# Performance work log

Hardware: AMD Instinct MI355X
Metric: run time of the kernel (lower is better)

The kernel has to match this reference:

```python
import math
import jax, jax.numpy as jnp
import numpy as np

N_HEAD = 16
N_HEAD_KV = 4
HEAD_DIM = 64
WINDOW = 512  # (window, 0) sliding-window causal, as in flash_attn window_size
ROPE_BASE = 10000.0


def _rope(x):
    """Rotate-half RoPE. x: (B, T, H, D)."""
    T, D = x.shape[1], x.shape[3]
    half = D // 2
    inv_freq = 1.0 / (ROPE_BASE ** (jnp.arange(half, dtype=jnp.float32) / half))
    ang = jnp.arange(T, dtype=jnp.float32)[:, None] * inv_freq[None, :]  # (T, half)
    cos = jnp.concatenate([jnp.cos(ang), jnp.cos(ang)], axis=-1)[None, :, None, :]
    sin = jnp.concatenate([jnp.sin(ang), jnp.sin(ang)], axis=-1)[None, :, None, :]
    x1, x2 = jnp.split(x, 2, axis=-1)
    rot = jnp.concatenate([-x2, x1], axis=-1)
    return x * cos.astype(x.dtype) + rot * sin.astype(x.dtype)


def setup_inputs() -> dict:
    key = jax.random.key(0)
    ks = jax.random.split(key, 7)
    B, T, C = 2, 2048, 1024
    Ckv = N_HEAD_KV * HEAD_DIM
    x = jax.random.normal(ks[0], (B, T, C), dtype=jnp.float32)
    seq_lengths = jax.random.randint(ks[1], (B,), T // 2, T + 1, dtype=jnp.int32)
    s = 0.02
    Wq = jax.random.normal(ks[2], (C, C), dtype=jnp.float32) * s
    Wk = jax.random.normal(ks[3], (C, Ckv), dtype=jnp.float32) * s
    Wv = jax.random.normal(ks[4], (C, Ckv), dtype=jnp.float32) * s
    Wo = jax.random.normal(ks[5], (C, C), dtype=jnp.float32) * s
    return {"x": x, "seq_lengths": seq_lengths, "Wq": Wq, "Wk": Wk, "Wv": Wv, "Wo": Wo}


def reference(x, seq_lengths, Wq, Wk, Wv, Wo):
    B, T, C = x.shape
    scale = 1.0 / math.sqrt(HEAD_DIM)
    q = (x @ Wq).reshape(B, T, N_HEAD, HEAD_DIM)
    k = (x @ Wk).reshape(B, T, N_HEAD_KV, HEAD_DIM)
    v = (x @ Wv).reshape(B, T, N_HEAD_KV, HEAD_DIM)
    q = _rope(q)
    k = _rope(k)
    # GQA: repeat_interleave KV heads up to N_HEAD
    rep = N_HEAD // N_HEAD_KV
    k = jnp.repeat(k, rep, axis=2)
    v = jnp.repeat(v, rep, axis=2)
    scores = jnp.einsum("bqhd,bkhd->bhqk", q, k) * scale  # (B,H,T,T)
    pos = jnp.arange(T)
    causal = pos[None, :] <= pos[:, None]                      # k <= q
    window = pos[None, :] >= (pos[:, None] - WINDOW)           # k >= q - W
    key_valid = pos[None, :] < seq_lengths[:, None]            # (B,T)
    mask = (causal & window)[None, None, :, :] & key_valid[:, None, None, :]
    scores = jnp.where(mask, scores, jnp.float32(-1e9))
    attn = jax.nn.softmax(scores, axis=-1)
    out = jnp.einsum("bhqk,bkhd->bqhd", attn, v)
    # padded query positions are zeroed (pad_input semantics in the varlen path)
    q_valid = (pos[None, :] < seq_lengths[:, None]).astype(out.dtype)
    out = out * q_valid[:, :, None, None]
    return out.reshape(B, T, C) @ Wo
```

## Files before the change

kernel.cpp:

```cpp
#include <hip/hip_runtime.h>


using bf16x8 = __attribute__((ext_vector_type(8))) short;
using f32x4  = __attribute__((ext_vector_type(4))) float;

#define B_   2
#define T_   2048
#define H_   16
#define HKV_ 4
#define D_   64
#define WIN_ 512

#define QSCALE_ 0.18033688011112042f
#define LOG2_1E4_OVER32_ 0.41524101186092029f

__device__ __forceinline__ unsigned short f2b(float f) {
  union { float f; unsigned u; } v; v.f = f;
  unsigned r = v.u + 0x7FFFu + ((v.u >> 16) & 1u);
  return (unsigned short)(r >> 16);
}
__device__ __forceinline__ unsigned short f2b_fast(float f) {
  union { float f; unsigned u; } v; v.f = f;
  return (unsigned short)((v.u + 0x8000u) >> 16);
}

typedef const __attribute__((address_space(1))) void* gas_ptr;
typedef __attribute__((address_space(3))) void* las_ptr;
__device__ __forceinline__ void gl_lds16(const void* g, void* l) {
  __builtin_amdgcn_global_load_lds((gas_ptr)g, (las_ptr)l, 16, 0, 0);
}

__global__ __launch_bounds__(256) void prep_kernel(
    const float* __restrict__ x,
    const float* __restrict__ Wq, const float* __restrict__ Wk,
    const float* __restrict__ Wv, const float* __restrict__ Wo,
    unsigned short* __restrict__ xb,
    unsigned short* __restrict__ wqT, unsigned short* __restrict__ wkT,
    unsigned short* __restrict__ wvT, unsigned short* __restrict__ woT) {
  int bx = blockIdx.x;
  if (bx < 4096) {
    int i = bx * 256 + threadIdx.x;
    float4 v = ((const float4*)x)[i];
    ushort4 o; o.x = f2b(v.x); o.y = f2b(v.y); o.z = f2b(v.z); o.w = f2b(v.w);
    ((ushort4*)xb)[i] = o;
    return;
  }
  int id = bx - 4096;
  const float* W; unsigned short* WT; int N, n0, k0;
  if (id < 1024)      { W = Wq; WT = wqT; N = 1024; }
  else if (id < 2048) { W = Wo; WT = woT; N = 1024; id -= 1024; }
  else if (id < 2304) { W = Wk; WT = wkT; N = 256;  id -= 2048; }
  else                { W = Wv; WT = wvT; N = 256;  id -= 2304; }
  if (N == 1024) { n0 = (id & 31) * 32; k0 = (id >> 5) * 32; }
  else           { n0 = (id & 7)  * 32; k0 = (id >> 3) * 32; }
  __shared__ float tile[32][33];
  int tx = threadIdx.x & 31, ty = threadIdx.x >> 5;
#pragma unroll
  for (int yy = 0; yy < 32; yy += 8)
    tile[ty + yy][tx] = W[(size_t)(k0 + ty + yy) * N + n0 + tx];
  __syncthreads();
#pragma unroll
  for (int yy = 0; yy < 32; yy += 8)
    WT[(size_t)(n0 + ty + yy) * 1024 + k0 + tx] = f2b(tile[tx][ty + yy]);
}

__global__ __launch_bounds__(256) void gemm_qkv(
    const unsigned short* __restrict__ A,
    const unsigned short* __restrict__ WqT,
    const unsigned short* __restrict__ WkT,
    const unsigned short* __restrict__ WvT,
    unsigned short* __restrict__ qb,
    unsigned short* __restrict__ kbuf,
    unsigned short* __restrict__ vbT) {
  const int K = 1024;
  __shared__ unsigned short lA[2][64 * 32];
  __shared__ unsigned short lB[2][128 * 32];
  int tid = threadIdx.x, l = tid & 63, w = tid >> 6;
  int wr = w >> 1, wc = w & 1;
  int m0 = blockIdx.x * 64;
  int n0 = blockIdx.y * 128;
  const unsigned short* Bt; int nloc;
  if (n0 < 1024)      { Bt = WqT; nloc = n0; }
  else if (n0 < 1280) { Bt = WkT; nloc = n0 - 1024; }
  else                { Bt = WvT; nloc = n0 - 1280; }

  f32x4 acc[2][4] = {};

  const unsigned short* ga = A  + (size_t)(m0   + w * 16 + (l >> 2)) * K + (l & 3) * 8;
  const unsigned short* gb = Bt + (size_t)(nloc + w * 16 + (l >> 2)) * K + (l & 3) * 8;

#define STG(BUF, KOFF)                                                        \
  { gl_lds16(ga + (KOFF),                  &lA[BUF][w * 512]);                \
    gl_lds16(gb + (KOFF),                  &lB[BUF][w * 512]);                \
    gl_lds16(gb + (size_t)64 * K + (KOFF), &lB[BUF][w * 512 + 2048]); }

  STG(0, 0)
  __syncthreads();
  for (int k0 = 0; k0 < K; k0 += 32) {
    int buf = (k0 >> 5) & 1;
    if (k0 + 32 < K) STG(buf ^ 1, k0 + 32)
    bf16x8 af[2], bfr[4];
#pragma unroll
    for (int mf = 0; mf < 2; ++mf)
      af[mf] = *(const bf16x8*)(&lA[buf][(wr * 32 + mf * 16 + (l & 15)) * 32 + (l >> 4) * 8]);
#pragma unroll
    for (int nf = 0; nf < 4; ++nf)
      bfr[nf] = *(const bf16x8*)(&lB[buf][(wc * 64 + nf * 16 + (l & 15)) * 32 + (l >> 4) * 8]);
#pragma unroll
    for (int mf = 0; mf < 2; ++mf)
#pragma unroll
      for (int nf = 0; nf < 4; ++nf)
        acc[mf][nf] = __builtin_amdgcn_mfma_f32_16x16x32_bf16(af[mf], bfr[nf], acc[mf][nf], 0, 0, 0);
    __syncthreads();
  }
#undef STG

  int colbase = n0 + wc * 64;
  int rowbase = m0 + wr * 32;

  if (n0 < 1280) {
    float qs = (n0 < 1024) ? QSCALE_ : 1.0f;
#pragma unroll
    for (int nf = 0; nf < 2; ++nf) {
      int dd = nf * 16 + (l & 15);
      float inv = exp2f(-(float)dd * LOG2_1E4_OVER32_);
#pragma unroll
      for (int mf = 0; mf < 2; ++mf) {
#pragma unroll
        for (int i = 0; i < 4; ++i) {
          int t = (rowbase + mf * 16 + ((l >> 4) << 2) + i) & 2047;
          float sn, cs;
          __sincosf((float)t * inv, &sn, &cs);
          float x1 = acc[mf][nf][i], x2 = acc[mf][nf + 2][i];
          acc[mf][nf][i]     = (x1 * cs - x2 * sn) * qs;
          acc[mf][nf + 2][i] = (x2 * cs + x1 * sn) * qs;
        }
      }
    }
  }

#pragma unroll
  for (int mf = 0; mf < 2; ++mf)
#pragma unroll
    for (int nf = 0; nf < 4; ++nf) {
      int n    = colbase + nf * 16 + (l & 15);
      int mrow = rowbase + mf * 16 + ((l >> 4) << 2);
      int b = mrow >> 11, t = mrow & 2047;
      if (n < 1024) {
        int h = n >> 6, d = n & 63;
        size_t base = ((size_t)(b * 16 + h) * 2048 + t) * 64 + d;
#pragma unroll
        for (int i = 0; i < 4; ++i) qb[base + (size_t)i * 64] = f2b(acc[mf][nf][i]);
      } else if (n < 1280) {
        int hh = (n - 1024) >> 6, d = n & 63;
        size_t base = ((size_t)(b * 4 + hh) * 2048 + t) * 64 + d;
#pragma unroll
        for (int i = 0; i < 4; ++i) kbuf[base + (size_t)i * 64] = f2b(acc[mf][nf][i]);
      } else {
        int hh = (n - 1280) >> 6, d = n & 63;
        size_t base = ((size_t)((b * 4 + hh) * 64 + d)) * 2048 + t;
        ushort4 pk;
        pk.x = f2b(acc[mf][nf][0]); pk.y = f2b(acc[mf][nf][1]);
        pk.z = f2b(acc[mf][nf][2]); pk.w = f2b(acc[mf][nf][3]);
        *(ushort4*)(&vbT[base]) = pk;
      }
    }
}

__global__ __launch_bounds__(512, 4) void attn_kernel(
    const unsigned short* __restrict__ qb,
    const unsigned short* __restrict__ kb,
    const unsigned short* __restrict__ vbT,
    const int* __restrict__ seqlen,
    unsigned short* __restrict__ att) {
  __shared__ unsigned short kl[2][64 * 64];
  __shared__ unsigned short vt[2][64 * 64];
  __shared__ unsigned short pl[8][16 * 68];

  int bx = blockIdx.x;
  int g  = bx & 7;
  int wi = bx >> 3;
  int b  = g >> 2;
  int hk = g & 3;
  int h  = hk * 4 + (wi & 3);
  int qt = wi >> 2;
  int tid = threadIdx.x, l = tid & 63, w = tid >> 6;
  int q0 = qt << 7;
  int r0 = q0 + w * 16;
  int slen = seqlen[b];

  const unsigned short* qbase = qb  + ((size_t)(b * 16 + h)  * 2048) * 64;
  const unsigned short* kbase = kb  + ((size_t)(b * 4  + hk) * 2048) * 64;
  const unsigned short* vbase = vbT + ((size_t)(b * 4  + hk) * 64)   * 2048;

  bf16x8 aq[2];
#pragma unroll
  for (int s = 0; s < 2; ++s)
    aq[s] = *(const bf16x8*)(qbase + (size_t)(r0 + (l & 15)) * 64 + s * 32 + (l >> 4) * 8);

  f32x4 o[4] = {};
  float lp[4] = {0.f, 0.f, 0.f, 0.f};

  int lo = q0 >= WIN_ ? q0 - WIN_ : 0;
  int nt = (q0 + 128 - lo) >> 6;

  int srow = (w << 3) + (l >> 3);
  int scol = (((l & 7) ^ (l >> 3)) << 3);
  const unsigned short* ksrc = kbase + (size_t)srow * 64   + scol;
  const unsigned short* vsrc = vbase + (size_t)srow * 2048 + scol;

#define STAGE(BUF, KB0)                                                        \
  {                                                                            \
    gl_lds16(ksrc + (size_t)(KB0) * 64, &kl[BUF][w * 512]);                    \
    gl_lds16(vsrc + (KB0),              &vt[BUF][w * 512]);                    \
  }

  STAGE(0, lo)
  __syncthreads();

  for (int it = 0; it < nt; ++it) {
    int kb0 = lo + (it << 6);
    int cur = it & 1;
    if (it + 1 < nt) STAGE(cur ^ 1, kb0 + 64)

    if (kb0 <= r0 + 15 && kb0 + 63 >= r0 - WIN_) {
      f32x4 sa[4];
      __builtin_amdgcn_s_setprio(1);
#pragma unroll
      for (int nf = 0; nf < 4; ++nf) {
        int row = nf * 16 + (l & 15);
        const unsigned short* kp0 =
            &kl[cur][row * 64 + (((l >> 4)       ^ (l & 7)) << 3)];
        const unsigned short* kp1 =
            &kl[cur][row * 64 + (((4 + (l >> 4)) ^ (l & 7)) << 3)];
        f32x4 z = {};
        z = __builtin_amdgcn_mfma_f32_16x16x32_bf16(aq[0], *(const bf16x8*)kp0, z, 0, 0, 0);
        z = __builtin_amdgcn_mfma_f32_16x16x32_bf16(aq[1], *(const bf16x8*)kp1, z, 0, 0, 0);
        sa[nf] = z;
      }
      __builtin_amdgcn_s_setprio(0);

      bool noMask = (kb0 + 63 <= r0) && (kb0 >= r0 - 497);
      if (!noMask) {
#pragma unroll
        for (int nf = 0; nf < 4; ++nf) {
          int key = kb0 + nf * 16 + (l & 15);
#pragma unroll
          for (int i = 0; i < 4; ++i) {
            int qr = r0 + (l >> 4) * 4 + i;
            sa[nf][i] = (key <= qr && key >= qr - WIN_) ? sa[nf][i] : -1e30f;
          }
        }
      }

#pragma unroll
      for (int nf = 0; nf < 4; ++nf)
#pragma unroll
        for (int i = 0; i < 4; ++i) {
          float p = exp2f(sa[nf][i]);
          lp[i] += p;
          pl[w][((l >> 4) * 4 + i) * 68 + nf * 16 + (l & 15)] = f2b_fast(p);
        }

      bf16x8 ap0 = *(const bf16x8*)(&pl[w][(l & 15) * 68 + (l >> 4) * 8]);
      bf16x8 ap1 = *(const bf16x8*)(&pl[w][(l & 15) * 68 + 32 + (l >> 4) * 8]);

      __builtin_amdgcn_s_setprio(1);
#pragma unroll
      for (int df = 0; df < 4; ++df) {
        int row = df * 16 + (l & 15);
        const unsigned short* vp0 =
            &vt[cur][row * 64 + (((l >> 4)       ^ (l & 7)) << 3)];
        const unsigned short* vp1 =
            &vt[cur][row * 64 + (((4 + (l >> 4)) ^ (l & 7)) << 3)];
        o[df] = __builtin_amdgcn_mfma_f32_16x16x32_bf16(ap0, *(const bf16x8*)vp0, o[df], 0, 0, 0);
        o[df] = __builtin_amdgcn_mfma_f32_16x16x32_bf16(ap1, *(const bf16x8*)vp1, o[df], 0, 0, 0);
      }
      __builtin_amdgcn_s_setprio(0);
    }
    __syncthreads();
  }
#undef STAGE

#pragma unroll
  for (int off = 1; off <= 8; off <<= 1)
#pragma unroll
    for (int i = 0; i < 4; ++i)
      lp[i] += __shfl_xor(lp[i], off);

#pragma unroll
  for (int i = 0; i < 4; ++i) {
    int r = r0 + (l >> 4) * 4 + i;
    float inv = (r < slen && lp[i] > 0.f) ? 1.0f / lp[i] : 0.f;
#pragma unroll
    for (int df = 0; df < 4; ++df)
      att[((size_t)(b * 2048 + r)) * 1024 + h * 64 + df * 16 + (l & 15)] =
          f2b(o[df][i] * inv);
  }
}

__global__ __launch_bounds__(256) void gemm_out(
    const unsigned short* __restrict__ A,
    const unsigned short* __restrict__ Bt,
    float* __restrict__ C) {
  const int K = 1024;
  __shared__ unsigned short lA[2][64 * 32];
  __shared__ unsigned short lB[2][128 * 32];
  int tid = threadIdx.x, l = tid & 63, w = tid >> 6;
  int wr = w >> 1, wc = w & 1;
  int m0 = blockIdx.x * 64;
  int n0 = blockIdx.y * 128;

  f32x4 acc[2][4] = {};

  const unsigned short* ga = A  + (size_t)(m0 + w * 16 + (l >> 2)) * K + (l & 3) * 8;
  const unsigned short* gb = Bt + (size_t)(n0 + w * 16 + (l >> 2)) * K + (l & 3) * 8;

#define STG(BUF, KOFF)                                                        \
  { gl_lds16(ga + (KOFF),                  &lA[BUF][w * 512]);                \
    gl_lds16(gb + (KOFF),                  &lB[BUF][w * 512]);                \
    gl_lds16(gb + (size_t)64 * K + (KOFF), &lB[BUF][w * 512 + 2048]); }

  STG(0, 0)
  __syncthreads();
  for (int k0 = 0; k0 < K; k0 += 32) {
    int buf = (k0 >> 5) & 1;
    if (k0 + 32 < K) STG(buf ^ 1, k0 + 32)
    bf16x8 af[2], bfr[4];
#pragma unroll
    for (int mf = 0; mf < 2; ++mf)
      af[mf] = *(const bf16x8*)(&lA[buf][(wr * 32 + mf * 16 + (l & 15)) * 32 + (l >> 4) * 8]);
#pragma unroll
    for (int nf = 0; nf < 4; ++nf)
      bfr[nf] = *(const bf16x8*)(&lB[buf][(wc * 64 + nf * 16 + (l & 15)) * 32 + (l >> 4) * 8]);
#pragma unroll
    for (int mf = 0; mf < 2; ++mf)
#pragma unroll
      for (int nf = 0; nf < 4; ++nf)
        acc[mf][nf] = __builtin_amdgcn_mfma_f32_16x16x32_bf16(af[mf], bfr[nf], acc[mf][nf], 0, 0, 0);
    __syncthreads();
  }
#undef STG

  int colbase = n0 + wc * 64;
  int rowbase = m0 + wr * 32;
#pragma unroll
  for (int mf = 0; mf < 2; ++mf)
#pragma unroll
    for (int nf = 0; nf < 4; ++nf) {
      int n    = colbase + nf * 16 + (l & 15);
      int mrow = rowbase + mf * 16 + ((l >> 4) << 2);
#pragma unroll
      for (int i = 0; i < 4; ++i)
        C[(size_t)(mrow + i) * 1024 + n] = acc[mf][nf][i];
    }
}

extern "C" void kernel_launch(void* const* d_in, const int* in_sizes, int n_in,
                              void* d_out, int out_size, void* d_ws, size_t ws_size,
                              hipStream_t stream) {
  const float* x  = (const float*)d_in[0];
  const int*   sl = (const int*)d_in[1];
  const float* Wq = (const float*)d_in[2];
  const float* Wk = (const float*)d_in[3];
  const float* Wv = (const float*)d_in[4];
  const float* Wo = (const float*)d_in[5];
  float* out = (float*)d_out;

  char* p = (char*)d_ws;
  unsigned short* xb  = (unsigned short*)p; p += (size_t)4096 * 1024 * 2;
  unsigned short* wqT = (unsigned short*)p; p += (size_t)1024 * 1024 * 2;
  unsigned short* wkT = (unsigned short*)p; p += (size_t)256  * 1024 * 2;
  unsigned short* wvT = (unsigned short*)p; p += (size_t)256  * 1024 * 2;
  unsigned short* woT = (unsigned short*)p; p += (size_t)1024 * 1024 * 2;
  unsigned short* qb  = (unsigned short*)p; p += (size_t)B_ * H_   * T_ * D_ * 2;
  unsigned short* kbf = (unsigned short*)p; p += (size_t)B_ * HKV_ * T_ * D_ * 2;
  unsigned short* vbT = (unsigned short*)p; p += (size_t)B_ * HKV_ * D_ * T_ * 2;
  unsigned short* att = (unsigned short*)p; p += (size_t)4096 * 1024 * 2;

  prep_kernel<<<6656, 256, 0, stream>>>(x, Wq, Wk, Wv, Wo, xb, wqT, wkT, wvT, woT);
  gemm_qkv<<<dim3(64, 12), 256, 0, stream>>>(xb, wqT, wkT, wvT, qb, kbf, vbT);
  attn_kernel<<<512, 512, 0, stream>>>(qb, kbf, vbT, sl, att);
  gemm_out<<<dim3(64, 8), 256, 0, stream>>>(att, woT, out);
}
```

Baseline: 86.28 us.

## Deepen GEMM K-tile to 64 with XOR-swizzled LDS and explicit vmcnt pipelining

Both the QKV and output GEMMs now stage 64-wide K slices instead of 32, halving the number of loop iterations and barriers. The LDS layout gets an XOR swizzle on 16-byte chunks to avoid bank conflicts on the wider rows. Prefetch waits use explicit s_waitcnt vmcnt counts instead of a full __syncthreads, and s_setprio raises priority around the MFMA block. LDS usage doubles, which may lower occupancy, and the hand-tuned waitcnt relies on the compiler not reordering the async loads.

Result: faster. 69.47 us (-19.5%).

```diff
diff --git a/kernel.cpp b/kernel.cpp
--- a/kernel.cpp
+++ b/kernel.cpp
@@ -73,8 +73,8 @@
     unsigned short* __restrict__ kbuf,
     unsigned short* __restrict__ vbT) {
   const int K = 1024;
-  __shared__ unsigned short lA[2][64 * 32];
-  __shared__ unsigned short lB[2][128 * 32];
+  __shared__ unsigned short lA[2][64 * 64];
+  __shared__ unsigned short lB[2][128 * 64];
   int tid = threadIdx.x, l = tid & 63, w = tid >> 6;
   int wr = w >> 1, wc = w & 1;
   int m0 = blockIdx.x * 64;
@@ -86,32 +86,58 @@
 
   f32x4 acc[2][4] = {};
 
-  const unsigned short* ga = A  + (size_t)(m0   + w * 16 + (l >> 2)) * K + (l & 3) * 8;
-  const unsigned short* gb = Bt + (size_t)(nloc + w * 16 + (l >> 2)) * K + (l & 3) * 8;
-
-#define STG(BUF, KOFF)                                                        \
-  { gl_lds16(ga + (KOFF),                  &lA[BUF][w * 512]);                \
-    gl_lds16(gb + (KOFF),                  &lB[BUF][w * 512]);                \
-    gl_lds16(gb + (size_t)64 * K + (KOFF), &lB[BUF][w * 512 + 2048]); }
+  int scol = (((l & 7) ^ (l >> 3)) << 3);
+  const unsigned short* ga = A  + (size_t)(m0   + w * 16 + (l >> 3)) * K + scol;
+  const unsigned short* gb = Bt + (size_t)(nloc + w * 32 + (l >> 3)) * K + scol;
+
+#define STG(BUF, KOFF)                                                         \
+  {                                                                            \
+    gl_lds16(ga + (KOFF),                  &lA[BUF][(w * 16) * 64]);           \
+    gl_lds16(ga + 8 * K + (KOFF),          &lA[BUF][(w * 16 + 8) * 64]);       \
+    _Pragma("unroll")                                                          \
+    for (int j = 0; j < 4; ++j)                                                \
+      gl_lds16(gb + j * 8 * K + (KOFF),    &lB[BUF][(w * 32 + j * 8) * 64]);   \
+  }
 
   STG(0, 0)
-  __syncthreads();
-  for (int k0 = 0; k0 < K; k0 += 32) {
-    int buf = (k0 >> 5) & 1;
-    if (k0 + 32 < K) STG(buf ^ 1, k0 + 32)
-    bf16x8 af[2], bfr[4];
+  for (int it = 0; it < 16; ++it) {
+    int buf = it & 1;
+    if (it < 15) {
+      STG(buf ^ 1, (it + 1) * 64)
+      asm volatile("s_waitcnt vmcnt(6)" ::: "memory");
+    } else {
+      asm volatile("s_waitcnt vmcnt(0)" ::: "memory");
+    }
+    __builtin_amdgcn_sched_barrier(0);
+    __builtin_amdgcn_s_barrier();
+
+    bf16x8 af[2][2], bfr[4][2];
+#pragma unroll
+    for (int mf = 0; mf < 2; ++mf) {
+      int row = wr * 32 + mf * 16 + (l & 15);
+#pragma unroll
+      for (int ks = 0; ks < 2; ++ks)
+        af[mf][ks] = *(const bf16x8*)(
+            &lA[buf][row * 64 + (((ks * 4 + (l >> 4)) ^ (row & 7)) << 3)]);
+    }
+#pragma unroll
+    for (int nf = 0; nf < 4; ++nf) {
+      int row = wc * 64 + nf * 16 + (l & 15);
+#pragma unroll
+      for (int ks = 0; ks < 2; ++ks)
+        bfr[nf][ks] = *(const bf16x8*)(
+            &lB[buf][row * 64 + (((ks * 4 + (l >> 4)) ^ (row & 7)) << 3)]);
+    }
+    __builtin_amdgcn_s_setprio(1);
 #pragma unroll
     for (int mf = 0; mf < 2; ++mf)
-      af[mf] = *(const bf16x8*)(&lA[buf][(wr * 32 + mf * 16 + (l & 15)) * 32 + (l >> 4) * 8]);
-#pragma unroll
-    for (int nf = 0; nf < 4; ++nf)
-      bfr[nf] = *(const bf16x8*)(&lB[buf][(wc * 64 + nf * 16 + (l & 15)) * 32 + (l >> 4) * 8]);
-#pragma unroll
-    for (int mf = 0; mf < 2; ++mf)
-#pragma unroll
-      for (int nf = 0; nf < 4; ++nf)
-        acc[mf][nf] = __builtin_amdgcn_mfma_f32_16x16x32_bf16(af[mf], bfr[nf], acc[mf][nf], 0, 0, 0);
-    __syncthreads();
+#pragma unroll
+      for (int nf = 0; nf < 4; ++nf) {
+        acc[mf][nf] = __builtin_amdgcn_mfma_f32_16x16x32_bf16(af[mf][0], bfr[nf][0], acc[mf][nf], 0, 0, 0);
+        acc[mf][nf] = __builtin_amdgcn_mfma_f32_16x16x32_bf16(af[mf][1], bfr[nf][1], acc[mf][nf], 0, 0, 0);
+      }
+    __builtin_amdgcn_s_setprio(0);
+    __builtin_amdgcn_s_barrier();
   }
 #undef STG
 
@@ -304,8 +330,8 @@
     const unsigned short* __restrict__ Bt,
     float* __restrict__ C) {
   const int K = 1024;
-  __shared__ unsigned short lA[2][64 * 32];
-  __shared__ unsigned short lB[2][128 * 32];
+  __shared__ unsigned short lA[2][64 * 64];
+  __shared__ unsigned short lB[2][128 * 64];
   int tid = threadIdx.x, l = tid & 63, w = tid >> 6;
   int wr = w >> 1, wc = w & 1;
   int m0 = blockIdx.x * 64;
@@ -313,32 +339,58 @@
 
   f32x4 acc[2][4] = {};
 
-  const unsigned short* ga = A  + (size_t)(m0 + w * 16 + (l >> 2)) * K + (l & 3) * 8;
-  const unsigned short* gb = Bt + (size_t)(n0 + w * 16 + (l >> 2)) * K + (l & 3) * 8;
-
-#define STG(BUF, KOFF)                                                        \
-  { gl_lds16(ga + (KOFF),                  &lA[BUF][w * 512]);                \
-    gl_lds16(gb + (KOFF),                  &lB[BUF][w * 512]);                \
-    gl_lds16(gb + (size_t)64 * K + (KOFF), &lB[BUF][w * 512 + 2048]); }
+  int scol = (((l & 7) ^ (l >> 3)) << 3);
+  const unsigned short* ga = A  + (size_t)(m0 + w * 16 + (l >> 3)) * K + scol;
+  const unsigned short* gb = Bt + (size_t)(n0 + w * 32 + (l >> 3)) * K + scol;
+
+#define STG(BUF, KOFF)                                                         \
+  {                                                                            \
+    gl_lds16(ga + (KOFF),                  &lA[BUF][(w * 16) * 64]);           \
+    gl_lds16(ga + 8 * K + (KOFF),          &lA[BUF][(w * 16 + 8) * 64]);       \
+    _Pragma("unroll")                                                          \
+    for (int j = 0; j < 4; ++j)                                                \
+      gl_lds16(gb + j * 8 * K + (KOFF),    &lB[BUF][(w * 32 + j * 8) * 64]);   \
+  }
 
   STG(0, 0)
-  __syncthreads();
-  for (int k0 = 0; k0 < K; k0 += 32) {
-    int buf = (k0 >> 5) & 1;
-    if (k0 + 32 < K) STG(buf ^ 1, k0 + 32)
-    bf16x8 af[2], bfr[4];
+  for (int it = 0; it < 16; ++it) {
+    int buf = it & 1;
+    if (it < 15) {
+      STG(buf ^ 1, (it + 1) * 64)
+      asm volatile("s_waitcnt vmcnt(6)" ::: "memory");
+    } else {
+      asm volatile("s_waitcnt vmcnt(0)" ::: "memory");
+    }
+    __builtin_amdgcn_sched_barrier(0);
+    __builtin_amdgcn_s_barrier();
+
+    bf16x8 af[2][2], bfr[4][2];
+#pragma unroll
+    for (int mf = 0; mf < 2; ++mf) {
+      int row = wr * 32 + mf * 16 + (l & 15);
+#pragma unroll
+      for (int ks = 0; ks < 2; ++ks)
+        af[mf][ks] = *(const bf16x8*)(
+            &lA[buf][row * 64 + (((ks * 4 + (l >> 4)) ^ (row & 7)) << 3)]);
+    }
+#pragma unroll
+    for (int nf = 0; nf < 4; ++nf) {
+      int row = wc * 64 + nf * 16 + (l & 15);
+#pragma unroll
+      for (int ks = 0; ks < 2; ++ks)
+        bfr[nf][ks] = *(const bf16x8*)(
+            &lB[buf][row * 64 + (((ks * 4 + (l >> 4)) ^ (row & 7)) << 3)]);
+    }
+    __builtin_amdgcn_s_setprio(1);
 #pragma unroll
     for (int mf = 0; mf < 2; ++mf)
-      af[mf] = *(const bf16x8*)(&lA[buf][(wr * 32 + mf * 16 + (l & 15)) * 32 + (l >> 4) * 8]);
-#pragma unroll
-    for (int nf = 0; nf < 4; ++nf)
-      bfr[nf] = *(const bf16x8*)(&lB[buf][(wc * 64 + nf * 16 + (l & 15)) * 32 + (l >> 4) * 8]);
-#pragma unroll
-    for (int mf = 0; mf < 2; ++mf)
-#pragma unroll
-      for (int nf = 0; nf < 4; ++nf)
-        acc[mf][nf] = __builtin_amdgcn_mfma_f32_16x16x32_bf16(af[mf], bfr[nf], acc[mf][nf], 0, 0, 0);
-    __syncthreads();
+#pragma unroll
+      for (int nf = 0; nf < 4; ++nf) {
+        acc[mf][nf] = __builtin_amdgcn_mfma_f32_16x16x32_bf16(af[mf][0], bfr[nf][0], acc[mf][nf], 0, 0, 0);
+        acc[mf][nf] = __builtin_amdgcn_mfma_f32_16x16x32_bf16(af[mf][1], bfr[nf][1], acc[mf][nf], 0, 0, 0);
+      }
+    __builtin_amdgcn_s_setprio(0);
+    __builtin_amdgcn_s_barrier();
   }
 #undef STG
 
```
